# Kernel tuning notes

Measured on AMD Instinct MI355X. Metric: run time of the kernel, lower is better.

## Reference

```python
import jax, jax.numpy as jnp
import numpy as np
from jax import lax

B, W, M = 4, 20, 512
RNN_HID = 64
N_HIDDEN = RNN_HID          # bi = False
HALF = N_HIDDEN // 2
K = 10
LONG_K = W // 2             # conv_long kernel
LONG_OUT = W - 2 * (LONG_K - 1)   # = 2
N_SPATIAL = 10


def setup_inputs() -> dict:
    key = jax.random.key(0)
    ks = jax.random.split(key, 24)
    g = lambda i, shape, s=0.05: jax.random.normal(ks[i], shape, jnp.float32) * s
    return {
        "x": jax.random.normal(ks[0], (B, W, M), jnp.float32),
        # vanilla RNN (tanh), 1 layer, input_size=1
        "W_ih": g(1, (RNN_HID, 1), 0.2), "W_hh": g(2, (RNN_HID, RNN_HID), 0.1),
        "b_ih": g(3, (RNN_HID,)), "b_hh": g(4, (RNN_HID,)),
        # attention adjacency params
        "W1": g(5, (HALF, N_HIDDEN), 0.1), "b1": g(6, (HALF,)),
        "W2": g(7, (HALF, N_HIDDEN), 0.1),
        "V": g(8, (HALF,), 0.1), "bv": g(9, (1,)),
        "Wb": g(10, (M, M), 0.05), "wb": g(11, (1,)),
        # conv / conv_long
        "conv_w": g(12, (K, 1, W), 0.1), "conv_b": g(13, (K,)),
        "convl_w": g(14, (K, 1, LONG_K), 0.1), "convl_b": g(15, (K,)),
        # graph conv layers: adj @ (x @ W) + b
        "gc1_w": g(16, ((1 + LONG_OUT) * K, N_HIDDEN), 0.1), "gc1_b": g(17, (N_HIDDEN,)),
        "gc2_w": g(18, (N_HIDDEN, N_SPATIAL), 0.1), "gc2_b": g(19, (N_SPATIAL,)),
        # output head
        "out_w": g(20, (1, N_HIDDEN + N_SPATIAL), 0.1), "out_b": g(21, (1,)),
        # fixed geographic adjacency (data.adj)
        "adj": jax.random.uniform(ks[22], (M, M), dtype=jnp.float32),
    }


def _conv1d(x, w, b, dilation=1):
    # x: (N, Cin, W), w: (Cout, Cin, K) -> (N, Cout, Wout), VALID padding
    y = lax.conv_general_dilated(x, w, (1,), 'VALID', rhs_dilation=(dilation,),
                                 dimension_numbers=('NCH', 'OIH', 'NCH'))
    return y + b[None, :, None]


def reference(x, W_ih, W_hh, b_ih, b_hh, W1, b1, W2, V, bv, Wb, wb,
              conv_w, conv_b, convl_w, convl_b, gc1_w, gc1_b, gc2_w, gc2_b,
              out_w, out_b, adj):
    b, w, m = x.shape
    # ---- RNN encode each node's scalar series: (b*m, w, 1) -> last hidden ----
    xr = jnp.transpose(x, (0, 2, 1)).reshape(b * m, w)          # (bm, w)
    inp = xr[..., None] @ W_ih.T + b_ih                         # (bm, w, H)

    def step(h, u):
        return jnp.tanh(u + h @ W_hh.T + b_hh), None

    h0 = jnp.zeros((b * m, RNN_HID), x.dtype)
    h_last, _ = lax.scan(step, h0, jnp.swapaxes(inp, 0, 1))     # (bm, H)
    last_hid = h_last.reshape(b, m, N_HIDDEN)
    out_temporal = last_hid

    # ---- pairwise bilinear attention adjacency (broadcast instead of repeat) ----
    p = last_hid @ W1.T                                         # (b, m, H/2)
    q = last_hid @ W2.T                                         # (b, m, H/2)
    e = jax.nn.elu(p[:, :, None, :] + q[:, None, :, :] + b1)    # (b, m, m, H/2)
    a_mx = e @ V + bv[0]                                        # (b, m, m)
    # F.normalize(p=2, dim=1)
    nrm = jnp.maximum(jnp.sqrt(jnp.sum(a_mx * a_mx, axis=1, keepdims=True)), 1e-12)
    a_mx = a_mx / nrm
    c = jax.nn.sigmoid(a_mx @ Wb + wb[0])                       # (b, m, m)
    A = adj[None] * c + a_mx * (1.0 - c)

    # ---- per-node convs, batched over all b*m series (no Python loop) ----
    h_tmp = xr[:, None, :]                                      # (bm, 1, w)
    r = _conv1d(h_tmp, conv_w, conv_b)                          # (bm, k, 1)
    r_long = _conv1d(h_tmp, convl_w, convl_b, dilation=2)       # (bm, k, long_out)
    r_l = jnp.concatenate([r, r_long], axis=-1).reshape(b, m, -1)  # (b, m, (1+lo)*k)
    r_l = jax.nn.relu(r_l)

    # ---- graph convolutions: adj @ (x @ W) + b ----
    xg = jax.nn.relu(A @ (r_l @ gc1_w) + gc1_b)                 # (b, m, H)
    out_spatial = jax.nn.relu(A @ (xg @ gc2_w) + gc2_b)         # (b, m, 10)

    out = jnp.concatenate([out_spatial, out_temporal], axis=-1)
    return (out @ out_w.T + out_b)[..., 0]                      # (b, m)
```

## Files before the change

### kernel.cpp

```cpp
#include <hip/hip_runtime.h>
#include <hip/hip_bf16.h>
#include <cstdint>
#include <cstddef>

#define OFF_P     0
#define OFF_QB    65536
#define OFF_TDOT  131072
#define OFF_COLSQ 133120
#define OFF_ZT    135168
#define OFF_G1B   155648
#define OFF_AMXB  221184
#define OFF_WBT   745472
#define OFF_ABF   1269760

typedef __attribute__((ext_vector_type(8))) short short8;
typedef __attribute__((ext_vector_type(8))) unsigned short ushort8;
typedef __attribute__((ext_vector_type(2))) unsigned short ushort2v;
typedef __attribute__((ext_vector_type(4))) float f32x4;

__device__ inline unsigned short f2bf(float f) {
    unsigned u = __builtin_bit_cast(unsigned, f);
    unsigned r = u + 0x7FFFu + ((u >> 16) & 1u);
    return (unsigned short)(r >> 16);
}
__device__ inline float bf2f(unsigned short s) {
    unsigned u = ((unsigned)s) << 16;
    return __builtin_bit_cast(float, u);
}
__device__ inline float tanh_fast(float x) {
    return 1.f - 2.f/(__expf(2.f*x) + 1.f);
}

__global__ __launch_bounds__(256) void k1_rnn(
    const float* __restrict__ x, const float* __restrict__ W_ih,
    const float* __restrict__ W_hh, const float* __restrict__ b_ih,
    const float* __restrict__ b_hh, const float* __restrict__ W1,
    const float* __restrict__ b1, const float* __restrict__ W2,
    const float* __restrict__ conv_w, const float* __restrict__ conv_b,
    const float* __restrict__ convl_w, const float* __restrict__ convl_b,
    const float* __restrict__ gc1_w, const float* __restrict__ out_w,
    const float* __restrict__ out_b,
    float* __restrict__ p_out, float* __restrict__ qb_out,
    unsigned short* __restrict__ G1bf, float* __restrict__ tdot,
    float* __restrict__ colsq)
{
    __shared__ float h_sh[4][64];
    __shared__ float xt_sh[4][20];
    __shared__ float rl_sh[4][30];
    int tid = threadIdx.x;
    int w = tid >> 6, lane = tid & 63;
    int s = blockIdx.x * 4 + w;
    int b = s >> 9, m = s & 511;

    if (blockIdx.x < 8) colsq[blockIdx.x * 256 + tid] = 0.f;

    if (lane < 20) xt_sh[w][lane] = x[(b*20 + lane)*512 + m];

    float wrow[64];
    const float* wr = W_hh + lane*64;
    #pragma unroll
    for (int k4 = 0; k4 < 16; ++k4) {
        float4 v = reinterpret_cast<const float4*>(wr)[k4];
        wrow[4*k4+0]=v.x; wrow[4*k4+1]=v.y; wrow[4*k4+2]=v.z; wrow[4*k4+3]=v.w;
    }
    float wih = W_ih[lane], bih = b_ih[lane], bhh = b_hh[lane];
    h_sh[w][lane] = 0.f;
    float h = 0.f;
    __syncthreads();

    for (int t = 0; t < 20; ++t) {
        float acc = xt_sh[w][t]*wih + bih + bhh;
        #pragma unroll
        for (int k = 0; k < 64; ++k) acc += wrow[k]*h_sh[w][k];
        h = tanh_fast(acc);
        __syncthreads();
        h_sh[w][lane] = h;
        __syncthreads();
    }

    float td = h * out_w[10 + lane];
    #pragma unroll
    for (int off = 32; off; off >>= 1) td += __shfl_down(td, off);
    if (lane == 0) tdot[s] = td + out_b[0];

    if (lane < 32) {
        const float* w1r = W1 + lane*64;
        float acc = 0.f;
        #pragma unroll
        for (int k = 0; k < 64; ++k) acc += w1r[k]*h_sh[w][k];
        p_out[s*32 + lane] = acc;
    } else {
        int i = lane - 32;
        const float* w2r = W2 + i*64;
        float acc = 0.f;
        #pragma unroll
        for (int k = 0; k < 64; ++k) acc += w2r[k]*h_sh[w][k];
        qb_out[s*32 + i] = acc + b1[i];
    }

    if (lane < 10) {
        float acc = conv_b[lane];
        #pragma unroll
        for (int t = 0; t < 20; ++t) acc += conv_w[lane*20+t]*xt_sh[w][t];
        rl_sh[w][3*lane] = fmaxf(acc, 0.f);
    } else if (lane < 30) {
        int idx = lane-10, j = idx>>1, oo = idx&1;
        float acc = convl_b[j];
        #pragma unroll
        for (int t = 0; t < 10; ++t) acc += convl_w[j*10+t]*xt_sh[w][oo+2*t];
        rl_sh[w][3*j+1+oo] = fmaxf(acc, 0.f);
    }
    __syncthreads();

    float g = 0.f;
    #pragma unroll
    for (int t = 0; t < 30; ++t) g += rl_sh[w][t]*gc1_w[t*64 + lane];
    G1bf[s*64 + lane] = f2bf(g);
}

__global__ __launch_bounds__(256) void k2_amx(
    const float* __restrict__ p, const float* __restrict__ qb,
    const float* __restrict__ V, const float* __restrict__ bv,
    unsigned short* __restrict__ amxB, float* __restrict__ colsq)
{
    __shared__ float p_sh[32*36], q_sh[32*36], v_sh[32], sq_sh[32*17];
    int t = threadIdx.x;
    int b = blockIdx.z, i0 = blockIdx.y*32, j0 = blockIdx.x*32;
    {
        int r = t >> 3, c4 = (t & 7)*4;
        *(float4*)&p_sh[r*36 + c4] = *(const float4*)(p  + (size_t)(b*512 + i0 + r)*32 + c4);
        *(float4*)&q_sh[r*36 + c4] = *(const float4*)(qb + (size_t)(b*512 + j0 + r)*32 + c4);
    }
    if (t < 32) v_sh[t] = V[t];
    __syncthreads();

    int ti = t >> 4, tj = t & 15;
    float bv0 = bv[0];
    float a00 = bv0, a01 = bv0, a10 = bv0, a11 = bv0;
    #pragma unroll
    for (int h = 0; h < 32; ++h) {
        float p0 = p_sh[ti*36 + h], p1 = p_sh[(ti+16)*36 + h];
        float q0 = q_sh[tj*36 + h], q1 = q_sh[(tj+16)*36 + h];
        float vh = v_sh[h];
        float x00 = p0+q0, x01 = p0+q1, x10 = p1+q0, x11 = p1+q1;
        float e00 = x00 > 0.f ? x00 : __expf(x00)-1.f;
        float e01 = x01 > 0.f ? x01 : __expf(x01)-1.f;
        float e10 = x10 > 0.f ? x10 : __expf(x10)-1.f;
        float e11 = x11 > 0.f ? x11 : __expf(x11)-1.f;
        a00 += vh*e00; a01 += vh*e01; a10 += vh*e10; a11 += vh*e11;
    }
    size_t base0 = ((size_t)(b*512 + i0 + ti))*512 + j0;
    size_t base1 = ((size_t)(b*512 + i0 + ti + 16))*512 + j0;
    amxB[base0 + tj]      = f2bf(a00);
    amxB[base0 + tj + 16] = f2bf(a01);
    amxB[base1 + tj]      = f2bf(a10);
    amxB[base1 + tj + 16] = f2bf(a11);

    sq_sh[tj*17 + ti]      = a00*a00 + a10*a10;
    sq_sh[(tj+16)*17 + ti] = a01*a01 + a11*a11;
    __syncthreads();
    if (t < 32) {
        float ssum = 0.f;
        #pragma unroll
        for (int r = 0; r < 16; ++r) ssum += sq_sh[t*17 + r];
        atomicAdd(&colsq[b*512 + j0 + t], ssum);
    }
}

__global__ __launch_bounds__(256) void k2w_scale(
    const float* __restrict__ Wb, const float* __restrict__ colsq,
    unsigned short* __restrict__ WbT)
{
    __shared__ float tile[64][68];
    int t = threadIdx.x;
    int j0 = blockIdx.x*64, k0 = blockIdx.y*64;
    #pragma unroll
    for (int q = 0; q < 4; ++q) {
        int kr = (t>>4) + 16*q;
        int jc = (t&15)*4;
        *(float4*)&tile[kr][jc] = *(const float4*)(Wb + (size_t)(k0+kr)*512 + j0 + jc);
    }
    __syncthreads();
    int jl = t>>2, kc = (t&3)*16;
    int j = j0 + jl;
    for (int b = 0; b < 4; ++b) {
        ushort8 v0, v1;
        #pragma unroll
        for (int kk = 0; kk < 8; ++kk) {
            float inv = 1.f/fmaxf(sqrtf(colsq[b*512 + k0+kc+kk]), 1e-12f);
            v0[kk] = f2bf(tile[kc+kk][jl] * inv);
        }
        #pragma unroll
        for (int kk = 0; kk < 8; ++kk) {
            float inv = 1.f/fmaxf(sqrtf(colsq[b*512 + k0+kc+8+kk]), 1e-12f);
            v1[kk] = f2bf(tile[kc+8+kk][jl] * inv);
        }
        unsigned short* dst = WbT + ((size_t)(b*512 + j))*512 + k0 + kc;
        *(ushort8*)dst = v0;
        *(ushort8*)(dst+8) = v1;
    }
}

__global__ __launch_bounds__(256) void k3a_mfma(
    const unsigned short* __restrict__ amxB, const unsigned short* __restrict__ WbT,
    const float* __restrict__ colsq, const float* __restrict__ wb,
    const float* __restrict__ adj, unsigned short* __restrict__ Abf)
{
    __shared__ __align__(16) unsigned short As[64*72];
    __shared__ __align__(16) unsigned short Bs[64*72];
    int t = threadIdx.x;
    int b = blockIdx.z;
    int i0 = blockIdx.y*64, j0 = blockIdx.x*64;
    int wv = t >> 6, lane = t & 63;
    int wr = (wv>>1)*32, wc = (wv&1)*32;
    f32x4 acc[2][2] = {};

    int srow = t >> 2, skc = (t&3)*16;
    const unsigned short* ag = amxB + ((size_t)(b*512 + i0 + srow))*512 + skc;
    const unsigned short* bg = WbT  + ((size_t)(b*512 + j0 + srow))*512 + skc;
    unsigned short* asl = &As[srow*72 + skc];
    unsigned short* bsl = &Bs[srow*72 + skc];

    for (int k0 = 0; k0 < 512; k0 += 64) {
        short8 a0 = *(const short8*)(ag + k0);
        short8 a1 = *(const short8*)(ag + k0 + 8);
        short8 b0 = *(const short8*)(bg + k0);
        short8 b1 = *(const short8*)(bg + k0 + 8);
        *(short8*)asl = a0; *(short8*)(asl+8) = a1;
        *(short8*)bsl = b0; *(short8*)(bsl+8) = b1;
        __syncthreads();
        #pragma unroll
        for (int h = 0; h < 2; ++h) {
            int kk = h*32 + (lane>>4)*8;
            short8 af0 = *(const short8*)&As[(wr +      (lane&15))*72 + kk];
            short8 af1 = *(const short8*)&As[(wr + 16 + (lane&15))*72 + kk];
            short8 bf0 = *(const short8*)&Bs[(wc +      (lane&15))*72 + kk];
            short8 bf1 = *(const short8*)&Bs[(wc + 16 + (lane&15))*72 + kk];
            acc[0][0] = __builtin_amdgcn_mfma_f32_16x16x32_bf16(af0, bf0, acc[0][0],0,0,0);
            acc[0][1] = __builtin_amdgcn_mfma_f32_16x16x32_bf16(af0, bf1, acc[0][1],0,0,0);
            acc[1][0] = __builtin_amdgcn_mfma_f32_16x16x32_bf16(af1, bf0, acc[1][0],0,0,0);
            acc[1][1] = __builtin_amdgcn_mfma_f32_16x16x32_bf16(af1, bf1, acc[1][1],0,0,0);
        }
        __syncthreads();
    }

    float wbs = wb[0];
    #pragma unroll
    for (int fj = 0; fj < 2; ++fj) {
        int j = j0 + wc + fj*16 + (lane&15);
        float inv = 1.f/fmaxf(sqrtf(colsq[b*512 + j]), 1e-12f);
        #pragma unroll
        for (int fi = 0; fi < 2; ++fi)
        #pragma unroll
        for (int r = 0; r < 4; ++r) {
            int i = i0 + wr + fi*16 + (lane>>4)*4 + r;
            float S = acc[fi][fj][r] + wbs;
            float c = 1.f/(1.f + __expf(-S));
            float aN = bf2f(amxB[((size_t)(b*512)+i)*512 + j]) * inv;
            Abf[((size_t)(b*512)+i)*512 + j] = f2bf(adj[i*512+j]*c + aN*(1.f - c));
        }
    }
}

#define G1T_STRIDE 536
__global__ __launch_bounds__(256) void k3b_mfma(
    const unsigned short* __restrict__ Abf, const unsigned short* __restrict__ G1bf,
    const float* __restrict__ gc1_b, const float* __restrict__ gc2_w,
    float* __restrict__ zT)
{
    __shared__ __align__(16) unsigned short G1T[64*G1T_STRIDE];
    __shared__ __align__(16) unsigned short As[64*72];
    __shared__ float xg[64*65];
    int t = threadIdx.x;
    int b = blockIdx.y, i0 = blockIdx.x*64;
    int wv = t >> 6, lane = t & 63;
    int wrow = wv*16;

    {
        int c = t & 63;
        int jg0 = t >> 6;
        for (int q = 0; q < 16; ++q) {
            int j0 = (jg0 + 4*q)*8;
            ushort8 v;
            #pragma unroll
            for (int jj = 0; jj < 8; ++jj)
                v[jj] = G1bf[((size_t)(b*512) + j0 + jj)*64 + c];
            *(ushort8*)&G1T[c*G1T_STRIDE + j0] = v;
        }
    }

    f32x4 acc[4] = {};
    int srow = t >> 2, skc = (t&3)*16;
    const unsigned short* ag = Abf + ((size_t)(b*512 + i0 + srow))*512 + skc;
    unsigned short* asl = &As[srow*72 + skc];
    __syncthreads();

    for (int k0 = 0; k0 < 512; k0 += 64) {
        short8 a0 = *(const short8*)(ag + k0);
        short8 a1 = *(const short8*)(ag + k0 + 8);
        *(short8*)asl = a0; *(short8*)(asl+8) = a1;
        __syncthreads();
        #pragma unroll
        for (int h = 0; h < 2; ++h) {
            int kk = h*32 + (lane>>4)*8;
            short8 af = *(const short8*)&As[(wrow + (lane&15))*72 + kk];
            #pragma unroll
            for (int cb = 0; cb < 4; ++cb) {
                short8 bfr = *(const short8*)&G1T[(cb*16 + (lane&15))*G1T_STRIDE + k0 + kk];
                acc[cb] = __builtin_amdgcn_mfma_f32_16x16x32_bf16(af, bfr, acc[cb],0,0,0);
            }
        }
        __syncthreads();
    }

    #pragma unroll
    for (int cb = 0; cb < 4; ++cb) {
        int c = cb*16 + (lane&15);
        float gb = gc1_b[c];
        #pragma unroll
        for (int r = 0; r < 4; ++r) {
            int row = wrow + (lane>>4)*4 + r;
            xg[row*65 + c] = fmaxf(acc[cb][r] + gb, 0.f);
        }
    }
    __syncthreads();

    {
        int rowz = t & 63;
        int sxb = t >> 6;
        #pragma unroll
        for (int kq = 0; kq < 3; ++kq) {
            int sx = sxb + 4*kq;
            if (sx < 10) {
                float a = 0.f;
                #pragma unroll
                for (int c = 0; c < 64; ++c) a += xg[rowz*65 + c]*gc2_w[c*10 + sx];
                zT[((size_t)(b*10) + sx)*512 + i0 + rowz] = a;
            }
        }
    }
}

__global__ __launch_bounds__(256) void k4_out(
    const unsigned short* __restrict__ Abf, const float* __restrict__ zT,
    const float* __restrict__ gc2_b, const float* __restrict__ out_w,
    const float* __restrict__ tdot, float* __restrict__ out)
{
    __shared__ float zt_l[5120];
    int t = threadIdx.x;
    int w = t >> 6, lane = t & 63;
    int s = blockIdx.x*4 + w;
    int b = s >> 9;
    #pragma unroll
    for (int q = 0; q < 20; ++q)
        zt_l[q*256 + t] = zT[(size_t)(b*5120) + q*256 + t];
    __syncthreads();

    const unsigned short* Arow = Abf + (size_t)s*512;
    float acc[10] = {};
    #pragma unroll
    for (int q = 0; q < 8; ++q) {
        int j = q*64 + lane;
        float a = bf2f(Arow[j]);
        #pragma unroll
        for (int sx = 0; sx < 10; ++sx) acc[sx] += a*zt_l[sx*512 + j];
    }
    #pragma unroll
    for (int sx = 0; sx < 10; ++sx)
        #pragma unroll
        for (int off = 32; off; off >>= 1) acc[sx] += __shfl_down(acc[sx], off);
    if (lane == 0) {
        float o = tdot[s];
        #pragma unroll
        for (int sx = 0; sx < 10; ++sx)
            o += fmaxf(acc[sx] + gc2_b[sx], 0.f) * out_w[sx];
        out[s] = o;
    }
}

extern "C" void kernel_launch(void* const* d_in, const int* in_sizes, int n_in,
                              void* d_out, int out_size, void* d_ws, size_t ws_size,
                              hipStream_t stream) {
    const float* x       = (const float*)d_in[0];
    const float* W_ih    = (const float*)d_in[1];
    const float* W_hh    = (const float*)d_in[2];
    const float* b_ih    = (const float*)d_in[3];
    const float* b_hh    = (const float*)d_in[4];
    const float* W1      = (const float*)d_in[5];
    const float* b1      = (const float*)d_in[6];
    const float* W2      = (const float*)d_in[7];
    const float* V       = (const float*)d_in[8];
    const float* bv      = (const float*)d_in[9];
    const float* Wb      = (const float*)d_in[10];
    const float* wb      = (const float*)d_in[11];
    const float* conv_w  = (const float*)d_in[12];
    const float* conv_b  = (const float*)d_in[13];
    const float* convl_w = (const float*)d_in[14];
    const float* convl_b = (const float*)d_in[15];
    const float* gc1_w   = (const float*)d_in[16];
    const float* gc1_b   = (const float*)d_in[17];
    const float* gc2_w   = (const float*)d_in[18];
    const float* gc2_b   = (const float*)d_in[19];
    const float* out_w   = (const float*)d_in[20];
    const float* out_b   = (const float*)d_in[21];
    const float* adj     = (const float*)d_in[22];

    float* ws    = (float*)d_ws;
    float* p     = ws + OFF_P;
    float* qb    = ws + OFF_QB;
    float* tdot  = ws + OFF_TDOT;
    float* colsq = ws + OFF_COLSQ;
    float* zT    = ws + OFF_ZT;
    unsigned short* G1bf = (unsigned short*)(ws + OFF_G1B);
    unsigned short* amxB = (unsigned short*)(ws + OFF_AMXB);
    unsigned short* WbT  = (unsigned short*)(ws + OFF_WBT);
    unsigned short* Abf  = (unsigned short*)(ws + OFF_ABF);
    float* out   = (float*)d_out;

    k1_rnn<<<dim3(512), dim3(256), 0, stream>>>(
        x, W_ih, W_hh, b_ih, b_hh, W1, b1, W2,
        conv_w, conv_b, convl_w, convl_b, gc1_w, out_w, out_b,
        p, qb, G1bf, tdot, colsq);

    k2_amx<<<dim3(16,16,4), dim3(256), 0, stream>>>(p, qb, V, bv, amxB, colsq);
    k2w_scale<<<dim3(8,8), dim3(256), 0, stream>>>(Wb, colsq, WbT);

    k3a_mfma<<<dim3(8,8,4), dim3(256), 0, stream>>>(amxB, WbT, colsq, wb, adj, Abf);
    k3b_mfma<<<dim3(8,4), dim3(256), 0, stream>>>(Abf, G1bf, gc1_b, gc2_w, zT);
    k4_out<<<dim3(512), dim3(256), 0, stream>>>(Abf, zT, gc2_b, out_w, tdot, out);
}
```

Before: 68.75 us.

## Drop RNN barriers, retile GEMM kernels and pre-transpose G1 for more parallelism

The RNN recurrence now relies on each wave owning one sequence, so the block-wide barriers are removed and the conv work moves before the loop. The Wb·amx GEMM switches to single-wave 32x32 tiles that load operands straight from global memory, with no LDS staging, across four times as many blocks. G1 is transposed once in extra blocks of the Wb scaling kernel, so the graph-conv GEMM can use 16-row tiles and launch 128 blocks instead of 32. The output kernel reads A and zT with vector loads instead of staging zT in LDS. The risks are that the barrier removal depends on wave-synchronous LDS ordering, and that the LDS-free GEMM may lose operand reuse.

```diff
diff --git a/kernel.cpp b/kernel.cpp
--- a/kernel.cpp
+++ b/kernel.cpp
@@ -12,10 +12,10 @@
 #define OFF_AMXB  221184
 #define OFF_WBT   745472
 #define OFF_ABF   1269760
+#define OFF_G1T   1794048
 
 typedef __attribute__((ext_vector_type(8))) short short8;
 typedef __attribute__((ext_vector_type(8))) unsigned short ushort8;
-typedef __attribute__((ext_vector_type(2))) unsigned short ushort2v;
 typedef __attribute__((ext_vector_type(4))) float f32x4;
 
 __device__ inline unsigned short f2bf(float f) {
@@ -66,16 +66,26 @@
     float wih = W_ih[lane], bih = b_ih[lane], bhh = b_hh[lane];
     h_sh[w][lane] = 0.f;
     float h = 0.f;
-    __syncthreads();
+
+    if (lane < 10) {
+        float acc = conv_b[lane];
+        #pragma unroll
+        for (int t = 0; t < 20; ++t) acc += conv_w[lane*20+t]*xt_sh[w][t];
+        rl_sh[w][3*lane] = fmaxf(acc, 0.f);
+    } else if (lane < 30) {
+        int idx = lane-10, j = idx>>1, oo = idx&1;
+        float acc = convl_b[j];
+        #pragma unroll
+        for (int t = 0; t < 10; ++t) acc += convl_w[j*10+t]*xt_sh[w][oo+2*t];
+        rl_sh[w][3*j+1+oo] = fmaxf(acc, 0.f);
+    }
 
     for (int t = 0; t < 20; ++t) {
         float acc = xt_sh[w][t]*wih + bih + bhh;
         #pragma unroll
         for (int k = 0; k < 64; ++k) acc += wrow[k]*h_sh[w][k];
         h = tanh_fast(acc);
-        __syncthreads();
         h_sh[w][lane] = h;
-        __syncthreads();
     }
 
     float td = h * out_w[10 + lane];
@@ -97,20 +107,6 @@
         for (int k = 0; k < 64; ++k) acc += w2r[k]*h_sh[w][k];
         qb_out[s*32 + i] = acc + b1[i];
     }
-
-    if (lane < 10) {
-        float acc = conv_b[lane];
-        #pragma unroll
-        for (int t = 0; t < 20; ++t) acc += conv_w[lane*20+t]*xt_sh[w][t];
-        rl_sh[w][3*lane] = fmaxf(acc, 0.f);
-    } else if (lane < 30) {
-        int idx = lane-10, j = idx>>1, oo = idx&1;
-        float acc = convl_b[j];
-        #pragma unroll
-        for (int t = 0; t < 10; ++t) acc += convl_w[j*10+t]*xt_sh[w][oo+2*t];
-        rl_sh[w][3*j+1+oo] = fmaxf(acc, 0.f);
-    }
-    __syncthreads();
 
     float g = 0.f;
     #pragma unroll
@@ -169,10 +165,42 @@
 
 __global__ __launch_bounds__(256) void k2w_scale(
     const float* __restrict__ Wb, const float* __restrict__ colsq,
-    unsigned short* __restrict__ WbT)
+    const unsigned short* __restrict__ G1bf,
+    unsigned short* __restrict__ WbT, unsigned short* __restrict__ G1T)
 {
     __shared__ float tile[64][68];
+    __shared__ unsigned short ttile[64*72];
     int t = threadIdx.x;
+
+    if (blockIdx.y == 8) {
+        int bb = blockIdx.x;
+        int b = bb >> 1;
+        int j0base = (bb & 1) * 256;
+        for (int chunk = 0; chunk < 4; ++chunk) {
+            int j0 = j0base + chunk*64;
+            {
+                int jr = t >> 2, c0 = (t & 3)*16;
+                const unsigned short* src = G1bf + ((size_t)(b*512 + j0 + jr))*64 + c0;
+                *(short8*)&ttile[jr*72 + c0]     = *(const short8*)src;
+                *(short8*)&ttile[jr*72 + c0 + 8] = *(const short8*)(src + 8);
+            }
+            __syncthreads();
+            {
+                int c = t >> 2, jc = (t & 3)*16;
+                ushort8 v0, v1;
+                #pragma unroll
+                for (int q = 0; q < 8; ++q) v0[q] = ttile[(jc+q)*72 + c];
+                #pragma unroll
+                for (int q = 0; q < 8; ++q) v1[q] = ttile[(jc+8+q)*72 + c];
+                unsigned short* dst = G1T + ((size_t)(b*64 + c))*512 + j0 + jc;
+                *(ushort8*)dst = v0;
+                *(ushort8*)(dst+8) = v1;
+            }
+            __syncthreads();
+        }
+        return;
+    }
+
     int j0 = blockIdx.x*64, k0 = blockIdx.y*64;
     #pragma unroll
     for (int q = 0; q < 4; ++q) {
@@ -201,59 +229,41 @@
     }
 }
 
-__global__ __launch_bounds__(256) void k3a_mfma(
+__global__ __launch_bounds__(64) void k3a_mfma(
     const unsigned short* __restrict__ amxB, const unsigned short* __restrict__ WbT,
     const float* __restrict__ colsq, const float* __restrict__ wb,
     const float* __restrict__ adj, unsigned short* __restrict__ Abf)
 {
-    __shared__ __align__(16) unsigned short As[64*72];
-    __shared__ __align__(16) unsigned short Bs[64*72];
-    int t = threadIdx.x;
+    int lane = threadIdx.x;
     int b = blockIdx.z;
-    int i0 = blockIdx.y*64, j0 = blockIdx.x*64;
-    int wv = t >> 6, lane = t & 63;
-    int wr = (wv>>1)*32, wc = (wv&1)*32;
+    int i0 = blockIdx.y*32, j0 = blockIdx.x*32;
     f32x4 acc[2][2] = {};
 
-    int srow = t >> 2, skc = (t&3)*16;
-    const unsigned short* ag = amxB + ((size_t)(b*512 + i0 + srow))*512 + skc;
-    const unsigned short* bg = WbT  + ((size_t)(b*512 + j0 + srow))*512 + skc;
-    unsigned short* asl = &As[srow*72 + skc];
-    unsigned short* bsl = &Bs[srow*72 + skc];
-
-    for (int k0 = 0; k0 < 512; k0 += 64) {
-        short8 a0 = *(const short8*)(ag + k0);
-        short8 a1 = *(const short8*)(ag + k0 + 8);
-        short8 b0 = *(const short8*)(bg + k0);
-        short8 b1 = *(const short8*)(bg + k0 + 8);
-        *(short8*)asl = a0; *(short8*)(asl+8) = a1;
-        *(short8*)bsl = b0; *(short8*)(bsl+8) = b1;
-        __syncthreads();
-        #pragma unroll
-        for (int h = 0; h < 2; ++h) {
-            int kk = h*32 + (lane>>4)*8;
-            short8 af0 = *(const short8*)&As[(wr +      (lane&15))*72 + kk];
-            short8 af1 = *(const short8*)&As[(wr + 16 + (lane&15))*72 + kk];
-            short8 bf0 = *(const short8*)&Bs[(wc +      (lane&15))*72 + kk];
-            short8 bf1 = *(const short8*)&Bs[(wc + 16 + (lane&15))*72 + kk];
-            acc[0][0] = __builtin_amdgcn_mfma_f32_16x16x32_bf16(af0, bf0, acc[0][0],0,0,0);
-            acc[0][1] = __builtin_amdgcn_mfma_f32_16x16x32_bf16(af0, bf1, acc[0][1],0,0,0);
-            acc[1][0] = __builtin_amdgcn_mfma_f32_16x16x32_bf16(af1, bf0, acc[1][0],0,0,0);
-            acc[1][1] = __builtin_amdgcn_mfma_f32_16x16x32_bf16(af1, bf1, acc[1][1],0,0,0);
-        }
-        __syncthreads();
+    const unsigned short* abase = amxB + ((size_t)(b*512 + i0 + (lane&15)))*512 + (lane>>4)*8;
+    const unsigned short* bbase = WbT  + ((size_t)(b*512 + j0 + (lane&15)))*512 + (lane>>4)*8;
+
+    #pragma unroll 4
+    for (int k0 = 0; k0 < 512; k0 += 32) {
+        short8 a0 = *(const short8*)(abase + k0);
+        short8 a1 = *(const short8*)(abase + 16*512 + k0);
+        short8 b0 = *(const short8*)(bbase + k0);
+        short8 b1 = *(const short8*)(bbase + 16*512 + k0);
+        acc[0][0] = __builtin_amdgcn_mfma_f32_16x16x32_bf16(a0, b0, acc[0][0],0,0,0);
+        acc[0][1] = __builtin_amdgcn_mfma_f32_16x16x32_bf16(a0, b1, acc[0][1],0,0,0);
+        acc[1][0] = __builtin_amdgcn_mfma_f32_16x16x32_bf16(a1, b0, acc[1][0],0,0,0);
+        acc[1][1] = __builtin_amdgcn_mfma_f32_16x16x32_bf16(a1, b1, acc[1][1],0,0,0);
     }
 
     float wbs = wb[0];
     #pragma unroll
     for (int fj = 0; fj < 2; ++fj) {
-        int j = j0 + wc + fj*16 + (lane&15);
+        int j = j0 + fj*16 + (lane&15);
         float inv = 1.f/fmaxf(sqrtf(colsq[b*512 + j]), 1e-12f);
         #pragma unroll
         for (int fi = 0; fi < 2; ++fi)
         #pragma unroll
         for (int r = 0; r < 4; ++r) {
-            int i = i0 + wr + fi*16 + (lane>>4)*4 + r;
+            int i = i0 + fi*16 + (lane>>4)*4 + r;
             float S = acc[fi][fj][r] + wbs;
             float c = 1.f/(1.f + __expf(-S));
             float aN = bf2f(amxB[((size_t)(b*512)+i)*512 + j]) * inv;
@@ -262,82 +272,53 @@
     }
 }
 
-#define G1T_STRIDE 536
+#define AS_STRIDE 520
 __global__ __launch_bounds__(256) void k3b_mfma(
-    const unsigned short* __restrict__ Abf, const unsigned short* __restrict__ G1bf,
+    const unsigned short* __restrict__ Abf, const unsigned short* __restrict__ G1T,
     const float* __restrict__ gc1_b, const float* __restrict__ gc2_w,
     float* __restrict__ zT)
 {
-    __shared__ __align__(16) unsigned short G1T[64*G1T_STRIDE];
-    __shared__ __align__(16) unsigned short As[64*72];
-    __shared__ float xg[64*65];
+    __shared__ __align__(16) unsigned short As[16*AS_STRIDE];
+    __shared__ float xg[16][68];
     int t = threadIdx.x;
-    int b = blockIdx.y, i0 = blockIdx.x*64;
+    int b = blockIdx.y, i0 = blockIdx.x*16;
     int wv = t >> 6, lane = t & 63;
-    int wrow = wv*16;
 
     {
-        int c = t & 63;
-        int jg0 = t >> 6;
-        for (int q = 0; q < 16; ++q) {
-            int j0 = (jg0 + 4*q)*8;
-            ushort8 v;
-            #pragma unroll
-            for (int jj = 0; jj < 8; ++jj)
-                v[jj] = G1bf[((size_t)(b*512) + j0 + jj)*64 + c];
-            *(ushort8*)&G1T[c*G1T_STRIDE + j0] = v;
-        }
-    }
-
-    f32x4 acc[4] = {};
-    int srow = t >> 2, skc = (t&3)*16;
-    const unsigned short* ag = Abf + ((size_t)(b*512 + i0 + srow))*512 + skc;
-    unsigned short* asl = &As[srow*72 + skc];
+        int r = t >> 4, seg = (t & 15)*32;
+        const unsigned short* src = Abf + ((size_t)(b*512 + i0 + r))*512 + seg;
+        *(short8*)&As[r*AS_STRIDE + seg]      = *(const short8*)src;
+        *(short8*)&As[r*AS_STRIDE + seg + 8]  = *(const short8*)(src + 8);
+        *(short8*)&As[r*AS_STRIDE + seg + 16] = *(const short8*)(src + 16);
+        *(short8*)&As[r*AS_STRIDE + seg + 24] = *(const short8*)(src + 24);
+    }
     __syncthreads();
 
-    for (int k0 = 0; k0 < 512; k0 += 64) {
-        short8 a0 = *(const short8*)(ag + k0);
-        short8 a1 = *(const short8*)(ag + k0 + 8);
-        *(short8*)asl = a0; *(short8*)(asl+8) = a1;
-        __syncthreads();
-        #pragma unroll
-        for (int h = 0; h < 2; ++h) {
-            int kk = h*32 + (lane>>4)*8;
-            short8 af = *(const short8*)&As[(wrow + (lane&15))*72 + kk];
-            #pragma unroll
-            for (int cb = 0; cb < 4; ++cb) {
-                short8 bfr = *(const short8*)&G1T[(cb*16 + (lane&15))*G1T_STRIDE + k0 + kk];
-                acc[cb] = __builtin_amdgcn_mfma_f32_16x16x32_bf16(af, bfr, acc[cb],0,0,0);
-            }
-        }
-        __syncthreads();
-    }
-
-    #pragma unroll
-    for (int cb = 0; cb < 4; ++cb) {
-        int c = cb*16 + (lane&15);
-        float gb = gc1_b[c];
-        #pragma unroll
-        for (int r = 0; r < 4; ++r) {
-            int row = wrow + (lane>>4)*4 + r;
-            xg[row*65 + c] = fmaxf(acc[cb][r] + gb, 0.f);
-        }
+    f32x4 acc = {};
+    const unsigned short* gbase = G1T + ((size_t)(b*64 + wv*16 + (lane&15)))*512 + (lane>>4)*8;
+    int aoff = (lane&15)*AS_STRIDE + (lane>>4)*8;
+    #pragma unroll 4
+    for (int k0 = 0; k0 < 512; k0 += 32) {
+        short8 af = *(const short8*)&As[aoff + k0];
+        short8 bf = *(const short8*)(gbase + k0);
+        acc = __builtin_amdgcn_mfma_f32_16x16x32_bf16(af, bf, acc, 0,0,0);
+    }
+
+    {
+        int cc = wv*16 + (lane&15);
+        float gb = gc1_b[cc];
+        #pragma unroll
+        for (int r = 0; r < 4; ++r)
+            xg[(lane>>4)*4 + r][cc] = fmaxf(acc[r] + gb, 0.f);
     }
     __syncthreads();
 
-    {
-        int rowz = t & 63;
-        int sxb = t >> 6;
-        #pragma unroll
-        for (int kq = 0; kq < 3; ++kq) {
-            int sx = sxb + 4*kq;
-            if (sx < 10) {
-                float a = 0.f;
-                #pragma unroll
-                for (int c = 0; c < 64; ++c) a += xg[rowz*65 + c]*gc2_w[c*10 + sx];
-                zT[((size_t)(b*10) + sx)*512 + i0 + rowz] = a;
-            }
-        }
+    if (t < 160) {
+        int row = t/10, sx = t%10;
+        float a = 0.f;
+        #pragma unroll
+        for (int c = 0; c < 64; ++c) a += xg[row][c]*gc2_w[c*10 + sx];
+        zT[((size_t)(b*10) + sx)*512 + i0 + row] = a;
     }
 }
 
@@ -346,24 +327,24 @@
     const float* __restrict__ gc2_b, const float* __restrict__ out_w,
     const float* __restrict__ tdot, float* __restrict__ out)
 {
-    __shared__ float zt_l[5120];
     int t = threadIdx.x;
     int w = t >> 6, lane = t & 63;
     int s = blockIdx.x*4 + w;
     int b = s >> 9;
-    #pragma unroll
-    for (int q = 0; q < 20; ++q)
-        zt_l[q*256 + t] = zT[(size_t)(b*5120) + q*256 + t];
-    __syncthreads();
-
-    const unsigned short* Arow = Abf + (size_t)s*512;
-    float acc[10] = {};
-    #pragma unroll
-    for (int q = 0; q < 8; ++q) {
-        int j = q*64 + lane;
-        float a = bf2f(Arow[j]);
-        #pragma unroll
-        for (int sx = 0; sx < 10; ++sx) acc[sx] += a*zt_l[sx*512 + j];
+
+    short8 av = *(const short8*)(Abf + (size_t)s*512 + lane*8);
+    float a[8];
+    #pragma unroll
+    for (int q = 0; q < 8; ++q) a[q] = bf2f((unsigned short)av[q]);
+
+    float acc[10];
+    #pragma unroll
+    for (int sx = 0; sx < 10; ++sx) {
+        const float* zr = zT + ((size_t)(b*10) + sx)*512 + lane*8;
+        float4 z0 = *(const float4*)zr;
+        float4 z1 = *(const float4*)(zr + 4);
+        acc[sx] = a[0]*z0.x + a[1]*z0.y + a[2]*z0.z + a[3]*z0.w
+                + a[4]*z1.x + a[5]*z1.y + a[6]*z1.z + a[7]*z1.w;
     }
     #pragma unroll
     for (int sx = 0; sx < 10; ++sx)
@@ -415,6 +396,7 @@
     unsigned short* amxB = (unsigned short*)(ws + OFF_AMXB);
     unsigned short* WbT  = (unsigned short*)(ws + OFF_WBT);
     unsigned short* Abf  = (unsigned short*)(ws + OFF_ABF);
+    unsigned short* G1T  = (unsigned short*)(ws + OFF_G1T);
     float* out   = (float*)d_out;
 
     k1_rnn<<<dim3(512), dim3(256), 0, stream>>>(
@@ -423,9 +405,9 @@
         p, qb, G1bf, tdot, colsq);
 
     k2_amx<<<dim3(16,16,4), dim3(256), 0, stream>>>(p, qb, V, bv, amxB, colsq);
-    k2w_scale<<<dim3(8,8), dim3(256), 0, stream>>>(Wb, colsq, WbT);
-
-    k3a_mfma<<<dim3(8,8,4), dim3(256), 0, stream>>>(amxB, WbT, colsq, wb, adj, Abf);
-    k3b_mfma<<<dim3(8,4), dim3(256), 0, stream>>>(Abf, G1bf, gc1_b, gc2_w, zT);
+    k2w_scale<<<dim3(8,9), dim3(256), 0, stream>>>(Wb, colsq, G1bf, WbT, G1T);
+
+    k3a_mfma<<<dim3(16,16,4), dim3(64), 0, stream>>>(amxB, WbT, colsq, wb, adj, Abf);
+    k3b_mfma<<<dim3(32,4), dim3(256), 0, stream>>>(Abf, G1T, gc1_b, gc2_w, zT);
     k4_out<<<dim3(512), dim3(256), 0, stream>>>(Abf, zT, gc2_b, out_w, tdot, out);
 }
```

Result: slower. 70.89 us (+3.1%).
